# Performance work log

Measured on AMD Instinct MI355X. Metric: run time of the kernel, lower is better.

The kernel has to match this reference:

```python
import jax, jax.numpy as jnp
import numpy as np

TAU = 250.0   # tau_inv used by all behaviours (norse default / explicit for LLBN)
DT = 0.001
VTH = 30.0
T_STEPS = 10000

# (a, b, c, d) Izhikevich params per cell
LLBN_P = (0.1, -0.075, -55.0, 6.0)      # custom spiking behaviour
EBN_P = (0.02, 0.25, -55.0, 0.05)       # phasic_bursting
IFN_P = (0.02, 0.25, -65.0, 6.0)        # phasic_spiking
TN_P = (0.02, 0.2, -65.0, 6.0)          # tonic_spiking
MN_P = (0.02, 0.25, -65.0, 6.0)         # phasic_spiking


def setup_inputs() -> dict:
    key = jax.random.key(0)
    k1, k2 = jax.random.split(key)
    input_mat = jax.random.uniform(k1, (127, 127), dtype=jnp.float32)
    weights_matrix = jax.random.uniform(k2, (12,), dtype=jnp.float32)
    return {"input_mat": input_mat, "weights_matrix": weights_matrix,
            "nb_repetitions": T_STEPS}


def _izh(v, u, I, p):
    a, b, c, d = p
    v1 = v + TAU * DT * (0.04 * v * v + 5.0 * v + 140.0 - u + I)
    u1 = u + TAU * DT * a * (b * v - u)
    z = (v1 >= VTH).astype(v.dtype)
    return z, jnp.where(z > 0, c, v1), u1 + z * d


def _simulate(input_mat, w, nb_repetitions):
    z_plus = jnp.sum(input_mat * w[0])  # constant across timesteps

    def step(carry, _):
        temp, z2p, v2, u2, v3, u3, v4, u4, z5p, v5, u5, v6, u6 = carry
        # LLBN: recurrent cell, input current = w2*(z_plus*w1 - temp) + w3*z_prev
        z2, v2, u2 = _izh(v2, u2, w[2] * (z_plus * w[1] - temp) + w[3] * z2p, LLBN_P)
        # EBN
        z3, v3, u3 = _izh(v3, u3, z_plus * w[4] + z2 * w[5], EBN_P)
        # IFN (feedback to LLBN via temp, one-step delay)
        z4, v4, u4 = _izh(v4, u4, z3 * w[6], IFN_P)
        temp_n = z4 * w[7]
        # TN: recurrent cell, input current = w9*(z3*w8) + w10*z_prev
        z5, v5, u5 = _izh(v5, u5, w[9] * (z3 * w[8]) + w[10] * z5p, TN_P)
        # MN
        z6, v6, u6 = _izh(v6, u6, z5 * w[11], MN_P)
        new_carry = (temp_n, z2, v2, u2, v3, u3, v4, u4, z5, v5, u5, v6, u6)
        out = (jnp.stack([z2, z3, z4, z5, z6]),  # spikes [5]
               jnp.stack([v2, v3, v4, v5, v6]))  # membrane voltages [5]
        return new_carry, out

    f32 = jnp.float32
    init = (f32(0.0),                      # temp
            f32(0.0), f32(-60.0), f32(4.5),    # LLBN z, v, u (u0 = b*v_rest)
            f32(-64.0), f32(-16.0),            # EBN v, u
            f32(-64.0), f32(-16.0),            # IFN v, u
            f32(0.0), f32(-70.0), f32(-14.0),  # TN z, v, u
            f32(-64.0), f32(-16.0))            # MN v, u
    _, (spikes, volts) = jax.lax.scan(step, init, None, length=nb_repetitions)
    return spikes.T, volts.T  # each [5, T]


def reference(input_mat, weights_matrix, nb_repetitions):
    o_spikes, v = _simulate(input_mat, weights_matrix, nb_repetitions)
    return o_spikes, v
```

## Files before the change

kernel.cpp:

```cpp
#include <hip/hip_runtime.h>

#pragma clang fp contract(off)


__device__ __forceinline__ float sel_mask(float a, float b, unsigned long long m) {
    float r;
    asm("v_cndmask_b32 %0, %1, %2, %3" : "=v"(r) : "v"(a), "v"(b), "s"(m));
    return r;
}

__global__ __launch_bounds__(256) void net_sim(const float* __restrict__ mat,
                                               const float* __restrict__ w,
                                               float* __restrict__ out,
                                               int* __restrict__ ws,
                                               int T) {
    __shared__ double red[256];
    const int tid = threadIdx.x;

    const float w0 = w[0];
    double s = 0.0;
    for (int i = tid; i < 127 * 127; i += 256) {
        float p = mat[i] * w0;
        s += (double)p;
    }
    red[tid] = s;
    __syncthreads();
    #pragma unroll
    for (int off = 128; off > 0; off >>= 1) {
        if (tid < off) red[tid] += red[tid + off];
        __syncthreads();
    }
    if (tid >= 9) return;

    const float z_plus = (float)red[0];

    const float w2 = w[2], w3 = w[3], w5 = w[5], w6 = w[6], w7 = w[7],
                w8 = w[8], w9 = w[9], w10 = w[10], w11 = w[11];
    const float zp_w1 = z_plus * w[1];
    const float zp_w4 = z_plus * w[4];

    const float I2_00 = w2 * (zp_w1 - 0.0f) + w3 * 0.0f;
    const float I2_10 = w2 * (zp_w1 - 0.0f) + w3 * 1.0f;
    const float I2_01 = w2 * (zp_w1 - w7)   + w3 * 0.0f;
    const float I2_11 = w2 * (zp_w1 - w7)   + w3 * 1.0f;
    const float I3_0  = zp_w4 + 0.0f * w5;
    const float I3_1  = zp_w4 + 1.0f * w5;
    const float I4_0  = 0.0f * w6;
    const float I4_1  = 1.0f * w6;
    const float I5_00 = w9 * (0.0f * w8) + w10 * 0.0f;
    const float I5_10 = w9 * (1.0f * w8) + w10 * 0.0f;
    const float I5_01 = w9 * (0.0f * w8) + w10 * 1.0f;
    const float I5_11 = w9 * (1.0f * w8) + w10 * 1.0f;
    const float I6_0  = 0.0f * w11;
    const float I6_1  = 1.0f * w11;

    const int lane = tid;
    const int g = lane == 0 ? 0 : lane <= 2 ? 1 : lane <= 4 ? 2 : lane <= 6 ? 3 : 4;

    const float ka = lane == 0 ? (float)(0.25 * 0.1) : (float)(0.25 * 0.02);
    const float b  = lane == 0 ? -0.075f : (g == 3 ? 0.2f : 0.25f);
    const float c  = g <= 1 ? -55.0f : -65.0f;
    const float d  = g == 1 ? 0.05f : 6.0f;
    float v = g == 0 ? -60.0f : (g == 3 ? -70.0f : -64.0f);
    float u = g == 0 ? 4.5f   : (g == 3 ? -14.0f : -16.0f);

    const float C0a = g == 0 ? I2_00 : g == 1 ? I3_0 : g == 2 ? I4_0
                    : g == 3 ? I5_00 : I6_0;
    const float C0b = g == 0 ? I2_00 : g == 1 ? I3_0 : g == 2 ? I4_0
                    : g == 3 ? I5_01 : I6_0;
    const float C1a = g == 1 ? I3_1 : g == 2 ? I4_1 : g == 3 ? I5_10
                    : g == 4 ? I6_1 : 0.0f;
    const float C1b = g == 1 ? I3_1 : g == 2 ? I4_1 : g == 3 ? I5_11
                    : g == 4 ? I6_1 : 0.0f;

    const bool is_lane0  = (lane == 0);
    const bool spec_var1 = (lane == 2) | (lane == 4) | (lane == 6) | (lane == 8);

    float* __restrict__ psp = out + g * T;
    float* __restrict__ pvv = out + 5 * T + g * T;

    int z2 = 0, z4 = 0, z5 = 0;

    float rav = 0.0f, rau = 0.0f; int raz2 = 0, raz4 = 0, raz5 = 0, ra_t = -1;
    float cav = 0.0f, cau = 0.0f; int caz2 = 0, caz4 = 0, caz5 = 0, ca_t = -1;
    int next_coarse = 8;
    int t_det = -1, Pf = 0;
    int blk5 = 0;

    float zb[8], vb[8];

    int t = 0;
    for (; t + 8 <= T; t += 8) {
        if (blk5 == 0) {
            if (ra_t >= 0) {
                unsigned long long mv =
                    __ballot(__float_as_uint(v) == __float_as_uint(rav));
                unsigned long long mu =
                    __ballot(__float_as_uint(u) == __float_as_uint(rau));
                if (((mv & mu) & 0x1FFull) == 0x1FFull &&
                    z2 == raz2 && z4 == raz4 && z5 == raz5) {
                    t_det = t; Pf = t - ra_t;
                    break;
                }
            }
            if (t) { rav = v; rau = u; raz2 = z2; raz4 = z4; raz5 = z5; ra_t = t; }
        } else if (ca_t >= 0) {
            unsigned long long mv =
                __ballot(__float_as_uint(v) == __float_as_uint(cav));
            unsigned long long mu =
                __ballot(__float_as_uint(u) == __float_as_uint(cau));
            if (((mv & mu) & 0x1FFull) == 0x1FFull &&
                z2 == caz2 && z4 == caz4 && z5 == caz5) {
                t_det = t; Pf = t - ca_t;
                break;
            }
        }
        if (t == next_coarse) {
            cav = v; cau = u; caz2 = z2; caz4 = z4; caz5 = z5; ca_t = t;
            next_coarse <<= 1;
        }
        blk5 = (blk5 == 4) ? 0 : (blk5 + 1);

        #pragma unroll
        for (int j = 0; j < 8; ++j) {
            float fI2 = z4 ? (z2 ? I2_11 : I2_01) : (z2 ? I2_10 : I2_00);
            float V0 = z5 ? C0b : C0a;
            float V1 = z5 ? C1b : C1a;
            V0 = is_lane0 ? fI2 : V0;
            float Ib = spec_var1 ? V1 : V0;

            float t1 = 0.04f * v;
            float t2 = t1 * v;
            float t3 = 5.0f * v;
            float t4 = t2 + t3;
            float t5 = t4 + 140.0f;
            float t6 = t5 - u;
            float bv = b * v;
            float bvu = bv - u;
            float du = ka * bvu;
            float u1 = u + du;

            float t7b = t6 + Ib;
            float v1b = fmaf(0.25f, t7b, v);
            unsigned long long m = __ballot(v1b >= 30.0f);

            int nz2 = (int)(m & 1ull);
            int z3  = (int)((m >> (1 + nz2)) & 1ull);
            int nz4 = (int)((m >> (3 + z3)) & 1ull);
            int nz5 = (int)((m >> (5 + z3)) & 1ull);
            unsigned long long ssel =
                (nz2 ? 0x006ull : 0ull) | (z3 ? 0x078ull : 0ull)
              | (nz5 ? 0x180ull : 0ull);

            float Ia = sel_mask(V0, V1, ssel);
            float t7a = t6 + Ia;
            float v1a = fmaf(0.25f, t7a, v);
            bool fa = (v1a >= 30.0f);
            v = fa ? c : v1a;
            float u1d = u1 + d;
            u = fa ? u1d : u1;

            zb[j] = fa ? 1.0f : 0.0f;
            vb[j] = v;

            z2 = nz2; z4 = nz4; z5 = nz5;
        }
        *(float4*)(psp)     = make_float4(zb[0], zb[1], zb[2], zb[3]);
        *(float4*)(psp + 4) = make_float4(zb[4], zb[5], zb[6], zb[7]);
        *(float4*)(pvv)     = make_float4(vb[0], vb[1], vb[2], vb[3]);
        *(float4*)(pvv + 4) = make_float4(vb[4], vb[5], vb[6], vb[7]);
        psp += 8;
        pvv += 8;
    }
    for (; t < T && t_det < 0; ++t) {
        float fI2 = z4 ? (z2 ? I2_11 : I2_01) : (z2 ? I2_10 : I2_00);
        float V0 = z5 ? C0b : C0a;
        float V1 = z5 ? C1b : C1a;
        V0 = is_lane0 ? fI2 : V0;
        float Ib = spec_var1 ? V1 : V0;
        float t1 = 0.04f * v;
        float t2 = t1 * v;
        float t3 = 5.0f * v;
        float t4 = t2 + t3;
        float t5 = t4 + 140.0f;
        float t6 = t5 - u;
        float bv = b * v;
        float bvu = bv - u;
        float du = ka * bvu;
        float u1 = u + du;
        float t7b = t6 + Ib;
        float v1b = fmaf(0.25f, t7b, v);
        unsigned long long m = __ballot(v1b >= 30.0f);
        int nz2 = (int)(m & 1ull);
        int z3  = (int)((m >> (1 + nz2)) & 1ull);
        int nz4 = (int)((m >> (3 + z3)) & 1ull);
        int nz5 = (int)((m >> (5 + z3)) & 1ull);
        unsigned long long ssel =
            (nz2 ? 0x006ull : 0ull) | (z3 ? 0x078ull : 0ull)
          | (nz5 ? 0x180ull : 0ull);
        float Ia = sel_mask(V0, V1, ssel);
        float t7a = t6 + Ia;
        float v1a = fmaf(0.25f, t7a, v);
        bool fa = (v1a >= 30.0f);
        v = fa ? c : v1a;
        float u1d = u1 + d;
        u = fa ? u1d : u1;
        psp[0] = fa ? 1.0f : 0.0f;
        pvv[0] = v;
        ++psp; ++pvv;
        z2 = nz2; z4 = nz4; z5 = nz5;
    }

    if (lane == 0) {
        ws[0] = (t_det >= 0) ? 1 : 0;
        ws[1] = t_det;
        ws[2] = Pf;
    }
}

__global__ __launch_bounds__(256) void fill_cycle(float* __restrict__ out,
                                                  const int* __restrict__ ws,
                                                  int T) {
    if (ws[0] == 0) return;
    const int t0 = ws[1];
    const int P  = ws[2];
    const int r  = blockIdx.y;
    const float* __restrict__ src = out + (size_t)r * T + (t0 - P);
    float* __restrict__ dst       = out + (size_t)r * T + t0;
    const int n = T - t0;
    for (int i = blockIdx.x * blockDim.x + threadIdx.x; i < n;
         i += gridDim.x * blockDim.x) {
        dst[i] = src[i % P];
    }
}

extern "C" void kernel_launch(void* const* d_in, const int* in_sizes, int n_in,
                              void* d_out, int out_size, void* d_ws, size_t ws_size,
                              hipStream_t stream) {
    const float* mat = (const float*)d_in[0];
    const float* w   = (const float*)d_in[1];
    int T = out_size / 10;
    net_sim<<<1, 256, 0, stream>>>(mat, w, (float*)d_out, (int*)d_ws, T);
    dim3 grid(40, 10, 1);
    fill_cycle<<<grid, 256, 0, stream>>>((float*)d_out, (const int*)d_ws, T);
}
```

Measured before the change: 293.3 us.

## Fuse cycle-fill into simulation kernel to remove second launch

The separate fill_cycle kernel is merged into net_sim: after the 9-lane simulation detects a period, the detection result is shared through LDS and all 256 threads of the single block replicate the periodic tail for all 10 rows. This removes a kernel launch and its dependency gap. The modulo is replaced by an incremental index. In exchange the fill now runs on a single block instead of 400 blocks, so filling a long tail gets much less memory parallelism.

```diff
diff --git a/kernel.cpp b/kernel.cpp
--- a/kernel.cpp
+++ b/kernel.cpp
@@ -15,6 +15,7 @@
                                                int* __restrict__ ws,
                                                int T) {
     __shared__ double red[256];
+    __shared__ int sdet[3];
     const int tid = threadIdx.x;
 
     const float w0 = w[0];
@@ -30,105 +31,159 @@
         if (tid < off) red[tid] += red[tid + off];
         __syncthreads();
     }
-    if (tid >= 9) return;
-
-    const float z_plus = (float)red[0];
-
-    const float w2 = w[2], w3 = w[3], w5 = w[5], w6 = w[6], w7 = w[7],
-                w8 = w[8], w9 = w[9], w10 = w[10], w11 = w[11];
-    const float zp_w1 = z_plus * w[1];
-    const float zp_w4 = z_plus * w[4];
-
-    const float I2_00 = w2 * (zp_w1 - 0.0f) + w3 * 0.0f;
-    const float I2_10 = w2 * (zp_w1 - 0.0f) + w3 * 1.0f;
-    const float I2_01 = w2 * (zp_w1 - w7)   + w3 * 0.0f;
-    const float I2_11 = w2 * (zp_w1 - w7)   + w3 * 1.0f;
-    const float I3_0  = zp_w4 + 0.0f * w5;
-    const float I3_1  = zp_w4 + 1.0f * w5;
-    const float I4_0  = 0.0f * w6;
-    const float I4_1  = 1.0f * w6;
-    const float I5_00 = w9 * (0.0f * w8) + w10 * 0.0f;
-    const float I5_10 = w9 * (1.0f * w8) + w10 * 0.0f;
-    const float I5_01 = w9 * (0.0f * w8) + w10 * 1.0f;
-    const float I5_11 = w9 * (1.0f * w8) + w10 * 1.0f;
-    const float I6_0  = 0.0f * w11;
-    const float I6_1  = 1.0f * w11;
-
-    const int lane = tid;
-    const int g = lane == 0 ? 0 : lane <= 2 ? 1 : lane <= 4 ? 2 : lane <= 6 ? 3 : 4;
-
-    const float ka = lane == 0 ? (float)(0.25 * 0.1) : (float)(0.25 * 0.02);
-    const float b  = lane == 0 ? -0.075f : (g == 3 ? 0.2f : 0.25f);
-    const float c  = g <= 1 ? -55.0f : -65.0f;
-    const float d  = g == 1 ? 0.05f : 6.0f;
-    float v = g == 0 ? -60.0f : (g == 3 ? -70.0f : -64.0f);
-    float u = g == 0 ? 4.5f   : (g == 3 ? -14.0f : -16.0f);
-
-    const float C0a = g == 0 ? I2_00 : g == 1 ? I3_0 : g == 2 ? I4_0
-                    : g == 3 ? I5_00 : I6_0;
-    const float C0b = g == 0 ? I2_00 : g == 1 ? I3_0 : g == 2 ? I4_0
-                    : g == 3 ? I5_01 : I6_0;
-    const float C1a = g == 1 ? I3_1 : g == 2 ? I4_1 : g == 3 ? I5_10
-                    : g == 4 ? I6_1 : 0.0f;
-    const float C1b = g == 1 ? I3_1 : g == 2 ? I4_1 : g == 3 ? I5_11
-                    : g == 4 ? I6_1 : 0.0f;
-
-    const bool is_lane0  = (lane == 0);
-    const bool spec_var1 = (lane == 2) | (lane == 4) | (lane == 6) | (lane == 8);
-
-    float* __restrict__ psp = out + g * T;
-    float* __restrict__ pvv = out + 5 * T + g * T;
-
-    int z2 = 0, z4 = 0, z5 = 0;
-
-    float rav = 0.0f, rau = 0.0f; int raz2 = 0, raz4 = 0, raz5 = 0, ra_t = -1;
-    float cav = 0.0f, cau = 0.0f; int caz2 = 0, caz4 = 0, caz5 = 0, ca_t = -1;
-    int next_coarse = 8;
-    int t_det = -1, Pf = 0;
-    int blk5 = 0;
-
-    float zb[8], vb[8];
-
-    int t = 0;
-    for (; t + 8 <= T; t += 8) {
-        if (blk5 == 0) {
-            if (ra_t >= 0) {
+
+    if (tid < 9) {
+        const float z_plus = (float)red[0];
+
+        const float w2 = w[2], w3 = w[3], w5 = w[5], w6 = w[6], w7 = w[7],
+                    w8 = w[8], w9 = w[9], w10 = w[10], w11 = w[11];
+        const float zp_w1 = z_plus * w[1];
+        const float zp_w4 = z_plus * w[4];
+
+        const float I2_00 = w2 * (zp_w1 - 0.0f) + w3 * 0.0f;
+        const float I2_10 = w2 * (zp_w1 - 0.0f) + w3 * 1.0f;
+        const float I2_01 = w2 * (zp_w1 - w7)   + w3 * 0.0f;
+        const float I2_11 = w2 * (zp_w1 - w7)   + w3 * 1.0f;
+        const float I3_0  = zp_w4 + 0.0f * w5;
+        const float I3_1  = zp_w4 + 1.0f * w5;
+        const float I4_0  = 0.0f * w6;
+        const float I4_1  = 1.0f * w6;
+        const float I5_00 = w9 * (0.0f * w8) + w10 * 0.0f;
+        const float I5_10 = w9 * (1.0f * w8) + w10 * 0.0f;
+        const float I5_01 = w9 * (0.0f * w8) + w10 * 1.0f;
+        const float I5_11 = w9 * (1.0f * w8) + w10 * 1.0f;
+        const float I6_0  = 0.0f * w11;
+        const float I6_1  = 1.0f * w11;
+
+        const int lane = tid;
+        const int g = lane == 0 ? 0 : lane <= 2 ? 1 : lane <= 4 ? 2
+                    : lane <= 6 ? 3 : 4;
+
+        const float ka = lane == 0 ? (float)(0.25 * 0.1) : (float)(0.25 * 0.02);
+        const float b  = lane == 0 ? -0.075f : (g == 3 ? 0.2f : 0.25f);
+        const float c  = g <= 1 ? -55.0f : -65.0f;
+        const float d  = g == 1 ? 0.05f : 6.0f;
+        float v = g == 0 ? -60.0f : (g == 3 ? -70.0f : -64.0f);
+        float u = g == 0 ? 4.5f   : (g == 3 ? -14.0f : -16.0f);
+
+        const float C0a = g == 0 ? I2_00 : g == 1 ? I3_0 : g == 2 ? I4_0
+                        : g == 3 ? I5_00 : I6_0;
+        const float C0b = g == 0 ? I2_00 : g == 1 ? I3_0 : g == 2 ? I4_0
+                        : g == 3 ? I5_01 : I6_0;
+        const float C1a = g == 1 ? I3_1 : g == 2 ? I4_1 : g == 3 ? I5_10
+                        : g == 4 ? I6_1 : 0.0f;
+        const float C1b = g == 1 ? I3_1 : g == 2 ? I4_1 : g == 3 ? I5_11
+                        : g == 4 ? I6_1 : 0.0f;
+
+        const bool is_lane0  = (lane == 0);
+        const bool spec_var1 = (lane == 2) | (lane == 4) | (lane == 6)
+                             | (lane == 8);
+
+        float* __restrict__ psp = out + g * T;
+        float* __restrict__ pvv = out + 5 * T + g * T;
+
+        int z2 = 0, z4 = 0, z5 = 0;
+
+        float rav = 0.0f, rau = 0.0f;
+        int raz2 = 0, raz4 = 0, raz5 = 0, ra_t = -1;
+        float cav = 0.0f, cau = 0.0f;
+        int caz2 = 0, caz4 = 0, caz5 = 0, ca_t = -1;
+        int next_coarse = 8;
+        int t_det = -1, Pf = 0;
+        int blk5 = 0;
+
+        float zb[8], vb[8];
+
+        int t = 0;
+        for (; t + 8 <= T; t += 8) {
+            if (blk5 == 0) {
+                if (ra_t >= 0) {
+                    unsigned long long mv =
+                        __ballot(__float_as_uint(v) == __float_as_uint(rav));
+                    unsigned long long mu =
+                        __ballot(__float_as_uint(u) == __float_as_uint(rau));
+                    if (((mv & mu) & 0x1FFull) == 0x1FFull &&
+                        z2 == raz2 && z4 == raz4 && z5 == raz5) {
+                        t_det = t; Pf = t - ra_t;
+                        break;
+                    }
+                }
+                if (t) { rav = v; rau = u; raz2 = z2; raz4 = z4; raz5 = z5;
+                         ra_t = t; }
+            } else if (ca_t >= 0) {
                 unsigned long long mv =
-                    __ballot(__float_as_uint(v) == __float_as_uint(rav));
+                    __ballot(__float_as_uint(v) == __float_as_uint(cav));
                 unsigned long long mu =
-                    __ballot(__float_as_uint(u) == __float_as_uint(rau));
+                    __ballot(__float_as_uint(u) == __float_as_uint(cau));
                 if (((mv & mu) & 0x1FFull) == 0x1FFull &&
-                    z2 == raz2 && z4 == raz4 && z5 == raz5) {
-                    t_det = t; Pf = t - ra_t;
+                    z2 == caz2 && z4 == caz4 && z5 == caz5) {
+                    t_det = t; Pf = t - ca_t;
                     break;
                 }
             }
-            if (t) { rav = v; rau = u; raz2 = z2; raz4 = z4; raz5 = z5; ra_t = t; }
-        } else if (ca_t >= 0) {
-            unsigned long long mv =
-                __ballot(__float_as_uint(v) == __float_as_uint(cav));
-            unsigned long long mu =
-                __ballot(__float_as_uint(u) == __float_as_uint(cau));
-            if (((mv & mu) & 0x1FFull) == 0x1FFull &&
-                z2 == caz2 && z4 == caz4 && z5 == caz5) {
-                t_det = t; Pf = t - ca_t;
-                break;
-            }
-        }
-        if (t == next_coarse) {
-            cav = v; cau = u; caz2 = z2; caz4 = z4; caz5 = z5; ca_t = t;
-            next_coarse <<= 1;
-        }
-        blk5 = (blk5 == 4) ? 0 : (blk5 + 1);
-
-        #pragma unroll
-        for (int j = 0; j < 8; ++j) {
+            if (t == next_coarse) {
+                cav = v; cau = u; caz2 = z2; caz4 = z4; caz5 = z5; ca_t = t;
+                next_coarse <<= 1;
+            }
+            blk5 = (blk5 == 4) ? 0 : (blk5 + 1);
+
+            #pragma unroll
+            for (int j = 0; j < 8; ++j) {
+                float fI2 = z4 ? (z2 ? I2_11 : I2_01) : (z2 ? I2_10 : I2_00);
+                float V0 = z5 ? C0b : C0a;
+                float V1 = z5 ? C1b : C1a;
+                V0 = is_lane0 ? fI2 : V0;
+                float Ib = spec_var1 ? V1 : V0;
+
+                float t1 = 0.04f * v;
+                float t2 = t1 * v;
+                float t3 = 5.0f * v;
+                float t4 = t2 + t3;
+                float t5 = t4 + 140.0f;
+                float t6 = t5 - u;
+                float bv = b * v;
+                float bvu = bv - u;
+                float du = ka * bvu;
+                float u1 = u + du;
+
+                float t7b = t6 + Ib;
+                float v1b = fmaf(0.25f, t7b, v);
+                unsigned long long m = __ballot(v1b >= 30.0f);
+
+                int nz2 = (int)(m & 1ull);
+                int z3  = (int)((m >> (1 + nz2)) & 1ull);
+                int nz4 = (int)((m >> (3 + z3)) & 1ull);
+                int nz5 = (int)((m >> (5 + z3)) & 1ull);
+                unsigned long long ssel =
+                    (nz2 ? 0x006ull : 0ull) | (z3 ? 0x078ull : 0ull)
+                  | (nz5 ? 0x180ull : 0ull);
+
+                float Ia = sel_mask(V0, V1, ssel);
+                float t7a = t6 + Ia;
+                float v1a = fmaf(0.25f, t7a, v);
+                bool fa = (v1a >= 30.0f);
+                v = fa ? c : v1a;
+                float u1d = u1 + d;
+                u = fa ? u1d : u1;
+
+                zb[j] = fa ? 1.0f : 0.0f;
+                vb[j] = v;
+
+                z2 = nz2; z4 = nz4; z5 = nz5;
+            }
+            *(float4*)(psp)     = make_float4(zb[0], zb[1], zb[2], zb[3]);
+            *(float4*)(psp + 4) = make_float4(zb[4], zb[5], zb[6], zb[7]);
+            *(float4*)(pvv)     = make_float4(vb[0], vb[1], vb[2], vb[3]);
+            *(float4*)(pvv + 4) = make_float4(vb[4], vb[5], vb[6], vb[7]);
+            psp += 8;
+            pvv += 8;
+        }
+        for (; t < T && t_det < 0; ++t) {
             float fI2 = z4 ? (z2 ? I2_11 : I2_01) : (z2 ? I2_10 : I2_00);
             float V0 = z5 ? C0b : C0a;
             float V1 = z5 ? C1b : C1a;
             V0 = is_lane0 ? fI2 : V0;
             float Ib = spec_var1 ? V1 : V0;
-
             float t1 = 0.04f * v;
             float t2 = t1 * v;
             float t3 = 5.0f * v;
@@ -139,11 +194,9 @@
             float bvu = bv - u;
             float du = ka * bvu;
             float u1 = u + du;
-
             float t7b = t6 + Ib;
             float v1b = fmaf(0.25f, t7b, v);
             unsigned long long m = __ballot(v1b >= 30.0f);
-
             int nz2 = (int)(m & 1ull);
             int z3  = (int)((m >> (1 + nz2)) & 1ull);
             int nz4 = (int)((m >> (3 + z3)) & 1ull);
@@ -151,7 +204,6 @@
             unsigned long long ssel =
                 (nz2 ? 0x006ull : 0ull) | (z3 ? 0x078ull : 0ull)
               | (nz5 ? 0x180ull : 0ull);
-
             float Ia = sel_mask(V0, V1, ssel);
             float t7a = t6 + Ia;
             float v1a = fmaf(0.25f, t7a, v);
@@ -159,78 +211,40 @@
             v = fa ? c : v1a;
             float u1d = u1 + d;
             u = fa ? u1d : u1;
-
-            zb[j] = fa ? 1.0f : 0.0f;
-            vb[j] = v;
-
+            psp[0] = fa ? 1.0f : 0.0f;
+            pvv[0] = v;
+            ++psp; ++pvv;
             z2 = nz2; z4 = nz4; z5 = nz5;
         }
-        *(float4*)(psp)     = make_float4(zb[0], zb[1], zb[2], zb[3]);
-        *(float4*)(psp + 4) = make_float4(zb[4], zb[5], zb[6], zb[7]);
-        *(float4*)(pvv)     = make_float4(vb[0], vb[1], vb[2], vb[3]);
-        *(float4*)(pvv + 4) = make_float4(vb[4], vb[5], vb[6], vb[7]);
-        psp += 8;
-        pvv += 8;
-    }
-    for (; t < T && t_det < 0; ++t) {
-        float fI2 = z4 ? (z2 ? I2_11 : I2_01) : (z2 ? I2_10 : I2_00);
-        float V0 = z5 ? C0b : C0a;
-        float V1 = z5 ? C1b : C1a;
-        V0 = is_lane0 ? fI2 : V0;
-        float Ib = spec_var1 ? V1 : V0;
-        float t1 = 0.04f * v;
-        float t2 = t1 * v;
-        float t3 = 5.0f * v;
-        float t4 = t2 + t3;
-        float t5 = t4 + 140.0f;
-        float t6 = t5 - u;
-        float bv = b * v;
-        float bvu = bv - u;
-        float du = ka * bvu;
-        float u1 = u + du;
-        float t7b = t6 + Ib;
-        float v1b = fmaf(0.25f, t7b, v);
-        unsigned long long m = __ballot(v1b >= 30.0f);
-        int nz2 = (int)(m & 1ull);
-        int z3  = (int)((m >> (1 + nz2)) & 1ull);
-        int nz4 = (int)((m >> (3 + z3)) & 1ull);
-        int nz5 = (int)((m >> (5 + z3)) & 1ull);
-        unsigned long long ssel =
-            (nz2 ? 0x006ull : 0ull) | (z3 ? 0x078ull : 0ull)
-          | (nz5 ? 0x180ull : 0ull);
-        float Ia = sel_mask(V0, V1, ssel);
-        float t7a = t6 + Ia;
-        float v1a = fmaf(0.25f, t7a, v);
-        bool fa = (v1a >= 30.0f);
-        v = fa ? c : v1a;
-        float u1d = u1 + d;
-        u = fa ? u1d : u1;
-        psp[0] = fa ? 1.0f : 0.0f;
-        pvv[0] = v;
-        ++psp; ++pvv;
-        z2 = nz2; z4 = nz4; z5 = nz5;
-    }
-
-    if (lane == 0) {
-        ws[0] = (t_det >= 0) ? 1 : 0;
-        ws[1] = t_det;
-        ws[2] = Pf;
-    }
-}
-
-__global__ __launch_bounds__(256) void fill_cycle(float* __restrict__ out,
-                                                  const int* __restrict__ ws,
-                                                  int T) {
-    if (ws[0] == 0) return;
-    const int t0 = ws[1];
-    const int P  = ws[2];
-    const int r  = blockIdx.y;
-    const float* __restrict__ src = out + (size_t)r * T + (t0 - P);
-    float* __restrict__ dst       = out + (size_t)r * T + t0;
-    const int n = T - t0;
-    for (int i = blockIdx.x * blockDim.x + threadIdx.x; i < n;
-         i += gridDim.x * blockDim.x) {
-        dst[i] = src[i % P];
+
+        if (lane == 0) {
+            ws[0] = (t_det >= 0) ? 1 : 0;
+            ws[1] = t_det;
+            ws[2] = Pf;
+            sdet[0] = (t_det >= 0) ? 1 : 0;
+            sdet[1] = t_det;
+            sdet[2] = Pf;
+        }
+    }
+
+    __syncthreads();
+    if (sdet[0]) {
+        const int t0 = sdet[1];
+        const int P  = sdet[2];
+        const int n  = T - t0;
+        if (n > 0) {
+            const int stp = 256 % P;
+            int k0 = tid % P;
+            for (int r = 0; r < 10; ++r) {
+                const float* __restrict__ src = out + (size_t)r * T + (t0 - P);
+                float* __restrict__ dst       = out + (size_t)r * T + t0;
+                int k = k0;
+                for (int i = tid; i < n; i += 256) {
+                    dst[i] = src[k];
+                    k += stp; if (k >= P) k -= P;
+                }
+            }
+        }
     }
 }
 
@@ -241,6 +255,4 @@
     const float* w   = (const float*)d_in[1];
     int T = out_size / 10;
     net_sim<<<1, 256, 0, stream>>>(mat, w, (float*)d_out, (int*)d_ws, T);
-    dim3 grid(40, 10, 1);
-    fill_cycle<<<grid, 256, 0, stream>>>((float*)d_out, (const int*)d_ws, T);
 }
```

New measurement: 335.2 us. 14.3% more time.
